# Optimization experiments

Hardware: AMD Instinct MI355X
Metric: run time of the kernel (lower is better)

Reference implementation:

```python
import jax, jax.numpy as jnp
import numpy as np

N = 50000
E = 800000
IN_C = 128
HID = 128
HEADS = 4
NEG_SLOPE = 0.2


def setup_inputs() -> dict:
    key = jax.random.key(0)
    ks = jax.random.split(key, 10)
    out_c = HID // HEADS  # 32
    glorot = lambda k, shape: jax.random.normal(k, shape, jnp.float32) * np.sqrt(2.0 / (shape[0] + shape[-1]))
    return {
        "x": jax.random.normal(ks[0], (N, IN_C), jnp.float32),
        "edge_index": jax.random.randint(ks[1], (2, E), 0, N, jnp.int64),
        # layer 1: GATConv(IN_C, out_c, heads=4, concat=True)
        "W1": glorot(ks[2], (IN_C, HEADS * out_c)),
        "att_src1": glorot(ks[3], (HEADS, out_c)),
        "att_dst1": glorot(ks[4], (HEADS, out_c)),
        "b1": jnp.zeros((HID,), jnp.float32),
        # layer 2: GATConv(HID, HID, heads=1, concat=False)
        "W2": glorot(ks[5], (HID, HID)),
        "att_src2": glorot(ks[6], (1, HID)),
        "att_dst2": glorot(ks[7], (1, HID)),
        "b2": jnp.zeros((HID,), jnp.float32),
    }


def _gat_conv(x, src, dst, W, att_src, att_dst, bias, heads, out_c):
    n = x.shape[0]
    h = (x @ W).reshape(n, heads, out_c)                 # [N, H, C]
    a_src = jnp.einsum("nhc,hc->nh", h, att_src)          # [N, H]
    a_dst = jnp.einsum("nhc,hc->nh", h, att_dst)          # [N, H]
    e = jax.nn.leaky_relu(a_src[src] + a_dst[dst], NEG_SLOPE)  # [E, H]
    # segment softmax over incoming edges of each dst node
    m = jax.ops.segment_max(e, dst, num_segments=n)
    p = jnp.exp(e - m[dst])
    denom = jax.ops.segment_sum(p, dst, num_segments=n)
    alpha = p / (denom[dst] + 1e-16)                      # [E, H]
    msg = h[src] * alpha[:, :, None]                      # [E, H, C]
    out = jax.ops.segment_sum(msg, dst, num_segments=n)   # [N, H, C]
    return out.reshape(n, heads * out_c) + bias


def reference(x, edge_index, W1, att_src1, att_dst1, b1, W2, att_src2, att_dst2, b2):
    n = x.shape[0]
    # PyG GATConv default add_self_loops=True
    loop = jnp.arange(n, dtype=edge_index.dtype)
    src = jnp.concatenate([edge_index[0], loop])
    dst = jnp.concatenate([edge_index[1], loop])

    out_c = HID // HEADS
    h = _gat_conv(x, src, dst, W1, att_src1, att_dst1, b1, HEADS, out_c)
    h = jax.nn.elu(h)  # dropout is identity in eval mode
    out = _gat_conv(h, src, dst, W2, att_src2, att_dst2, b2, 1, HID)
    return out
```

## Files before the change

### kernel.cpp

```cpp
#include <hip/hip_runtime.h>
#include <hip/hip_bf16.h>
#include <math.h>


#define NEG_SLOPE 0.2f
#define NBLK 256

using bf16x8 = __attribute__((ext_vector_type(8))) short;
using f32x4  = __attribute__((ext_vector_type(4))) float;

__device__ inline unsigned short f2bf(float x) {
    union { float f; unsigned int u; } v; v.f = x;
    unsigned int b = v.u + 0x7fffu + ((v.u >> 16) & 1u);
    return (unsigned short)(b >> 16);
}
__device__ inline unsigned int pack2bf(float a, float b) {
    return (unsigned int)f2bf(a) | ((unsigned int)f2bf(b) << 16);
}
__device__ inline float bf_lo(unsigned int u) { return __uint_as_float(u << 16); }
__device__ inline float bf_hi(unsigned int u) { return __uint_as_float(u & 0xffff0000u); }

__device__ inline int excl_scan_256(int v, int* scratch4) {
    const int t = threadIdx.x, lane = t & 63, w = t >> 6;
    int incl = v;
#pragma unroll
    for (int o = 1; o < 64; o <<= 1) {
        int u = __shfl_up(incl, o, 64);
        if (lane >= o) incl += u;
    }
    if (lane == 63) scratch4[w] = incl;
    __syncthreads();
    int wb = 0;
#pragma unroll
    for (int k = 0; k < 4; ++k)
        if (k < w) wb += scratch4[k];
    __syncthreads();
    return wb + incl - v;
}

__global__ __launch_bounds__(256) void part_hist_prep(const int* __restrict__ ei,
                                                      int* __restrict__ hist,
                                                      int E, int NB, int epb,
                                                      const float* __restrict__ W1,
                                                      const float* __restrict__ W2,
                                                      unsigned short* __restrict__ WT1,
                                                      unsigned short* __restrict__ WT2) {
    const int t = threadIdx.x;
    if (blockIdx.x >= NBLK) {
        __shared__ float Wl[64][132];
        const float* W = (blockIdx.x - NBLK) ? W2 : W1;
        unsigned short* WT = (blockIdx.x - NBLK) ? WT2 : WT1;
        for (int p = 0; p < 2; ++p) {
            if (p) __syncthreads();
            for (int u = t; u < 2048; u += 256) {
                int row = u >> 5, ch = u & 31;
                float4 v = *(const float4*)(W + (size_t)(p * 64 + row) * 128 + ch * 4);
                Wl[row][ch * 4 + 0] = v.x; Wl[row][ch * 4 + 1] = v.y;
                Wl[row][ch * 4 + 2] = v.z; Wl[row][ch * 4 + 3] = v.w;
            }
            __syncthreads();
            for (int u = t; u < 2048; u += 256) {
                int c = u >> 4, kc = u & 15;
                uint2 o;
                o.x = pack2bf(Wl[kc * 4 + 0][c], Wl[kc * 4 + 1][c]);
                o.y = pack2bf(Wl[kc * 4 + 2][c], Wl[kc * 4 + 3][c]);
                *(uint2*)(WT + (size_t)c * 128 + p * 64 + kc * 4) = o;
            }
        }
        return;
    }
    __shared__ int h[256];
    h[t] = 0;
    __syncthreads();
    const int e0 = blockIdx.x * epb;
    const int e1 = min(e0 + epb, E);
    for (int e = e0 + t; e < e1; e += 256) atomicAdd(&h[ei[E + e] >> 8], 1);
    __syncthreads();
    if (t < NB) hist[t * NBLK + blockIdx.x] = h[t];
}

__global__ __launch_bounds__(256) void part_scan(int* __restrict__ hist,
                                                 int* __restrict__ btotal) {
    __shared__ int s4[4];
    const int b = blockIdx.x, t = threadIdx.x;
    const int v = hist[b * NBLK + t];
    const int ex = excl_scan_256(v, s4);
    hist[b * NBLK + t] = ex;
    if (t == 255) btotal[b] = ex + v;
}

__global__ __launch_bounds__(256) void part_scatter(const int* __restrict__ ei,
                                                    const int* __restrict__ hist,
                                                    const int* __restrict__ btotal,
                                                    unsigned int* __restrict__ part,
                                                    int E, int NB, int epb) {
    __shared__ int s4[4];
    __shared__ int cur[256];
    const int t = threadIdx.x;
    const int tv = (t < NB) ? btotal[t] : 0;
    const int pb = excl_scan_256(tv, s4);
    cur[t] = (t < NB) ? pb + hist[t * NBLK + blockIdx.x] : 0;
    __syncthreads();
    const int e0 = blockIdx.x * epb;
    const int e1 = min(e0 + epb, E);
    for (int e = e0 + t; e < e1; e += 256) {
        const int d = ei[E + e];
        const int s = ei[e];
        const int pos = atomicAdd(&cur[d >> 8], 1);
        part[pos] = (unsigned int)s | ((unsigned int)(d & 255) << 16);
    }
}

__global__ __launch_bounds__(256) void csr_build(const unsigned int* __restrict__ part,
                                                 const int* __restrict__ btotal,
                                                 int* __restrict__ offs,
                                                 int* __restrict__ csr,
                                                 int n, int NB, int E) {
    __shared__ int s4[4];
    __shared__ int cnt[256], curq[256];
    __shared__ int sPB, sPE, sCB;
    const int b = blockIdx.x, t = threadIdx.x;
    const int tv = (t < NB) ? btotal[t] : 0;
    const int nnt = (t < NB) ? max(0, min(256, n - t * 256)) : 0;
    const int e1 = excl_scan_256(tv, s4);
    const int e2 = excl_scan_256(tv + nnt, s4);
    if (t == b) { sPB = e1; sPE = e1 + tv; sCB = e2; }
    const int node = b * 256 + t;
    cnt[t] = (node < n) ? 1 : 0;
    __syncthreads();
    for (int i = sPB + t; i < sPE; i += 256) atomicAdd(&cnt[(part[i] >> 16) & 255], 1);
    __syncthreads();
    const int c = cnt[t];
    const int loc = excl_scan_256(c, s4);
    curq[t] = loc + ((node < n) ? 1 : 0);
    if (node < n) {
        offs[node] = sCB + loc;
        csr[sCB + loc] = node;
    }
    if (b == 0 && t == 0) offs[n] = E + n;
    __syncthreads();
    for (int i = sPB + t; i < sPE; i += 256) {
        const unsigned int u = part[i];
        const int pos = atomicAdd(&curq[(u >> 16) & 255], 1);
        csr[sCB + pos] = (int)(u & 0xffffu);
    }
}

template <int H, bool IN_F32>
__global__ __launch_bounds__(512) void gemm_att(const float* __restrict__ Xf,
                                                const unsigned short* __restrict__ Xb,
                                                const unsigned short* __restrict__ WTb,
                                                unsigned int* __restrict__ Yb,
                                                const float* __restrict__ att_s,
                                                const float* __restrict__ att_d,
                                                float* __restrict__ as_,
                                                float* __restrict__ ad_, int n) {
    __shared__ unsigned short XL[128 * 128];
    __shared__ unsigned short WL[128 * 128];
    const int tid = threadIdx.x;
    const int r0g = blockIdx.x * 128;
#pragma unroll
    for (int p = 0; p < 4; ++p) {
        int u = tid + 512 * p;
        int row = u >> 4, ch = u & 15;
        uint4 v = {0, 0, 0, 0};
        int gr = r0g + row;
        if (gr < n) {
            if constexpr (IN_F32) {
                const float4* xp = (const float4*)(Xf + (size_t)gr * 128 + ch * 8);
                float4 f0 = xp[0], f1 = xp[1];
                v.x = pack2bf(f0.x, f0.y); v.y = pack2bf(f0.z, f0.w);
                v.z = pack2bf(f1.x, f1.y); v.w = pack2bf(f1.z, f1.w);
            } else {
                v = *(const uint4*)(Xb + (size_t)gr * 128 + ch * 8);
            }
        }
        int byte = (ch * 16) ^ ((row & 7) << 4);
        *(uint4*)((char*)XL + row * 256 + byte) = v;
    }
#pragma unroll
    for (int p = 0; p < 4; ++p) {
        int u = tid + 512 * p;
        int c = u >> 4, ch = u & 15;
        uint4 v = *(const uint4*)(WTb + (size_t)c * 128 + ch * 8);
        int byte = (ch * 16) ^ ((c & 7) << 4);
        *(uint4*)((char*)WL + c * 256 + byte) = v;
    }
    __syncthreads();

    const int w = tid >> 6, lane = tid & 63;
    const int lr = lane & 15, lq = lane >> 4;
    const int swz = (lr & 7) << 4;
    f32x4 acc[8];
#pragma unroll
    for (int cf = 0; cf < 8; ++cf) acc[cf] = (f32x4){0.f, 0.f, 0.f, 0.f};

    const char* XB = (const char*)XL + (w * 16 + lr) * 256;
    const char* WB = (const char*)WL + lr * 256;
#pragma unroll
    for (int k4 = 0; k4 < 4; ++k4) {
        const int off = (k4 * 64 + lq * 16) ^ swz;
        bf16x8 a = *(const bf16x8*)(XB + off);
#pragma unroll
        for (int cf = 0; cf < 8; ++cf) {
            bf16x8 b = *(const bf16x8*)(WB + cf * 4096 + off);
            acc[cf] = __builtin_amdgcn_mfma_f32_16x16x32_bf16(a, b, acc[cf], 0, 0, 0);
        }
    }

#pragma unroll
    for (int r = 0; r < 4; ++r) {
        int grow = r0g + w * 16 + lq * 4 + r;
        if (grow < n) {
            uint4 o;
            o.x = pack2bf(acc[0][r], acc[1][r]);
            o.y = pack2bf(acc[2][r], acc[3][r]);
            o.z = pack2bf(acc[4][r], acc[5][r]);
            o.w = pack2bf(acc[6][r], acc[7][r]);
            *(uint4*)((unsigned short*)Yb + (size_t)grow * 128 + lr * 8) = o;
        }
    }

    if constexpr (H == 4) {
        float pa[4][4], pd[4][4];
#pragma unroll
        for (int h = 0; h < 4; ++h)
#pragma unroll
            for (int r = 0; r < 4; ++r) { pa[h][r] = 0.f; pd[h][r] = 0.f; }
#pragma unroll
        for (int cf = 0; cf < 8; ++cf) {
            const float ws = att_s[cf * 16 + lr];
            const float wd = att_d[cf * 16 + lr];
#pragma unroll
            for (int r = 0; r < 4; ++r) {
                pa[cf >> 1][r] = fmaf(acc[cf][r], ws, pa[cf >> 1][r]);
                pd[cf >> 1][r] = fmaf(acc[cf][r], wd, pd[cf >> 1][r]);
            }
        }
#pragma unroll
        for (int o = 1; o < 16; o <<= 1) {
#pragma unroll
            for (int h = 0; h < 4; ++h)
#pragma unroll
                for (int r = 0; r < 4; ++r) {
                    pa[h][r] += __shfl_xor(pa[h][r], o, 64);
                    pd[h][r] += __shfl_xor(pd[h][r], o, 64);
                }
        }
        const int h = lr & 3, r = lr >> 2;
        float va = 0.f, vd = 0.f;
#pragma unroll
        for (int hh = 0; hh < 4; ++hh)
#pragma unroll
            for (int rr = 0; rr < 4; ++rr)
                if (h == hh && r == rr) { va = pa[hh][rr]; vd = pd[hh][rr]; }
        const int node = r0g + w * 16 + lq * 4 + r;
        if (node < n) {
            as_[(size_t)node * 4 + h] = va;
            ad_[(size_t)node * 4 + h] = vd;
        }
    } else {
        float pa[4], pd[4];
#pragma unroll
        for (int r = 0; r < 4; ++r) { pa[r] = 0.f; pd[r] = 0.f; }
#pragma unroll
        for (int cf = 0; cf < 8; ++cf) {
            const float ws = att_s[cf * 16 + lr];
            const float wd = att_d[cf * 16 + lr];
#pragma unroll
            for (int r = 0; r < 4; ++r) {
                pa[r] = fmaf(acc[cf][r], ws, pa[r]);
                pd[r] = fmaf(acc[cf][r], wd, pd[r]);
            }
        }
#pragma unroll
        for (int o = 1; o < 16; o <<= 1) {
#pragma unroll
            for (int r = 0; r < 4; ++r) {
                pa[r] += __shfl_xor(pa[r], o, 64);
                pd[r] += __shfl_xor(pd[r], o, 64);
            }
        }
        const int r = lr & 3;
        float va = 0.f, vd = 0.f;
#pragma unroll
        for (int rr = 0; rr < 4; ++rr)
            if (r == rr) { va = pa[rr]; vd = pd[rr]; }
        const int node = r0g + w * 16 + lq * 4 + r;
        if (node < n && lr < 8) {
            if (lr < 4) as_[node] = va;
            else        ad_[node] = vd;
        }
    }
}

template <int H, bool DO_ELU, bool OUT_BF16>
__global__ __launch_bounds__(256) void gat_gather5(
    const int* __restrict__ csr, const int* __restrict__ offs,
    const float* __restrict__ as_, const float* __restrict__ ad_,
    const unsigned int* __restrict__ hb,
    const float* __restrict__ bias, float* __restrict__ outf,
    unsigned short* __restrict__ outb, int n)
{
    constexpr int PW = (H == 4) ? 8 : 2;
    __shared__ float plds[4][68][PW];
    const int node = (int)(((size_t)blockIdx.x * blockDim.x + threadIdx.x) >> 6);
    if (node >= n) return;
    const int lane = threadIdx.x & 63;
    const int w = threadIdx.x >> 6;
    const int hd = lane & 3;
    const int lane4 = lane * 4;
    const int col0 = ((2 * lane) & 7) * 16 + (lane >> 2);
    const int col1 = col0 + 16;
    const int start = offs[node];
    const int deg = offs[node + 1] - start;
    const char* hbp = (const char*)hb;
    const char* pb = (const char*)&plds[w][0][0] + ((H == 4) ? hd * 8 : 0);

    if (lane < 3) {
#pragma unroll
        for (int k = 0; k < PW; ++k) plds[w][64 + lane][k] = 0.f;
    }

    float adx = 0.f, ady = 0.f, adz = 0.f, adw = 0.f;
    if constexpr (H == 4) {
        const float4 adv = *(const float4*)(ad_ + (size_t)node * 4);
        adx = adv.x; ady = adv.y; adz = adv.z; adw = adv.w;
    } else {
        adx = ad_[node];
    }

    float2 acc = {0.f, 0.f};
    float dsx = 0.f, dsy = 0.f, dsz = 0.f, dsw = 0.f;

    for (int base = 0; base < deg; base += 64) {
        const int cnt = min(deg - base, 64);
        {
            const bool act = lane < cnt;
            const int s = act ? csr[start + base + lane] : 0;
            const float sf = __int_as_float(s << 8);
            if constexpr (H == 4) {
                const float4 a = ((const float4*)as_)[s];
                float e0 = a.x + adx; e0 = fmaxf(e0, NEG_SLOPE * e0);
                float e1 = a.y + ady; e1 = fmaxf(e1, NEG_SLOPE * e1);
                float e2 = a.z + adz; e2 = fmaxf(e2, NEG_SLOPE * e2);
                float e3 = a.w + adw; e3 = fmaxf(e3, NEG_SLOPE * e3);
                float p0 = act ? __expf(e0) : 0.f;
                float p1 = act ? __expf(e1) : 0.f;
                float p2 = act ? __expf(e2) : 0.f;
                float p3 = act ? __expf(e3) : 0.f;
                dsx += p0; dsy += p1; dsz += p2; dsw += p3;
                float4 w0 = {p0, sf, p1, sf};
                float4 w1 = {p2, sf, p3, sf};
                *(float4*)&plds[w][lane][0] = w0;
                *(float4*)&plds[w][lane][4] = w1;
            } else {
                float e0 = as_[s] + adx; e0 = fmaxf(e0, NEG_SLOPE * e0);
                float p = act ? __expf(e0) : 0.f;
                dsx += p;
                float2 ps = {p, sf};
                *(float2*)&plds[w][lane][0] = ps;
            }
        }
        asm volatile("s_waitcnt lgkmcnt(0)" ::: "memory");
        __builtin_amdgcn_sched_barrier(0);

        float pA, pB, pC;
        unsigned int hA, hB, hC;
#define PRELB(S, T)                                                              \
    {                                                                            \
        const float2 ps = *(const float2*)(pb + (size_t)(T) * (PW * 4));         \
        p##S = ps.x;                                                             \
        h##S = *(const unsigned int*)(hbp + (__float_as_int(ps.y) | lane4));     \
    }
#define CONSB(S)                                                                 \
    {                                                                            \
        acc.x = fmaf(p##S, bf_lo(h##S), acc.x);                                  \
        acc.y = fmaf(p##S, bf_hi(h##S), acc.y);                                  \
    }
        PRELB(A, 0)
        PRELB(B, 1)
        PRELB(C, 2)
        int t = 0;
        for (; t + 3 <= cnt; t += 3) {
            CONSB(A) PRELB(A, t + 3)
            CONSB(B) PRELB(B, t + 4)
            CONSB(C) PRELB(C, t + 5)
        }
        if (t < cnt)     CONSB(A)
        if (t + 1 < cnt) CONSB(B)
        if (t + 2 < cnt) CONSB(C)
#undef PRELB
#undef CONSB
    }

#pragma unroll
    for (int o = 1; o < 64; o <<= 1) {
        dsx += __shfl_xor(dsx, o, 64);
        if constexpr (H == 4) {
            dsy += __shfl_xor(dsy, o, 64);
            dsz += __shfl_xor(dsz, o, 64);
            dsw += __shfl_xor(dsw, o, 64);
        }
    }
    float ds;
    if constexpr (H == 4) ds = hd == 0 ? dsx : hd == 1 ? dsy : hd == 2 ? dsz : dsw;
    else                  ds = dsx;

    const float bvx = bias[col0], bvy = bias[col1];
    const float inv = 1.f / (ds + 1e-16f);
    float v0 = acc.x * inv + bvx;
    float v1 = acc.y * inv + bvy;
    if constexpr (DO_ELU) {
        v0 = v0 > 0.f ? v0 : __expf(v0) - 1.f;
        v1 = v1 > 0.f ? v1 : __expf(v1) - 1.f;
    }
    if constexpr (OUT_BF16) {
        unsigned short* o16 = outb + (size_t)node * 128;
        o16[col0] = f2bf(v0);
        o16[col1] = f2bf(v1);
    } else {
        float* o32 = outf + (size_t)node * 128;
        o32[col0] = v0;
        o32[col1] = v1;
    }
}

extern "C" void kernel_launch(void* const* d_in, const int* in_sizes, int n_in,
                              void* d_out, int out_size, void* d_ws, size_t ws_size,
                              hipStream_t stream) {
    const float* x        = (const float*)d_in[0];
    const int*   ei       = (const int*)d_in[1];
    const float* W1       = (const float*)d_in[2];
    const float* att_src1 = (const float*)d_in[3];
    const float* att_dst1 = (const float*)d_in[4];
    const float* b1       = (const float*)d_in[5];
    const float* W2       = (const float*)d_in[6];
    const float* att_src2 = (const float*)d_in[7];
    const float* att_dst2 = (const float*)d_in[8];
    const float* b2       = (const float*)d_in[9];

    const int n  = in_sizes[0] / 128;
    const int E  = in_sizes[1] / 2;
    const int ET = E + n;
    const int NB = (n + 255) >> 8;
    const int epb = (E + NBLK - 1) / NBLK;

    unsigned int*   ws32 = (unsigned int*)d_ws;
    unsigned int*   Yb   = ws32;
    unsigned int*   Bb   = Yb + (size_t)n * 64;
    unsigned short* WT1  = (unsigned short*)(Bb + (size_t)n * 64);
    unsigned short* WT2  = WT1 + 128 * 128;
    float*          as_  = (float*)(WT2 + 128 * 128);
    float*          ad_  = as_ + (size_t)n * 4;
    int*            offs = (int*)(ad_ + (size_t)n * 4);
    int*            csr  = offs + n + 1;
    unsigned int*   part = (unsigned int*)(csr + ET);
    int*            hist = (int*)(part + E);
    int*            btot = hist + (size_t)NB * NBLK;

    float* outf = (float*)d_out;

    part_hist_prep<<<NBLK + 2, 256, 0, stream>>>(ei, hist, E, NB, epb,
                                                 W1, W2, WT1, WT2);
    part_scan<<<NB, 256, 0, stream>>>(hist, btot);
    part_scatter<<<NBLK, 256, 0, stream>>>(ei, hist, btot, part, E, NB, epb);
    csr_build<<<NB, 256, 0, stream>>>(part, btot, offs, csr, n, NB, E);

    gemm_att<4, true><<<(n + 127) / 128, 512, 0, stream>>>(
        x, nullptr, WT1, Yb, att_src1, att_dst1, as_, ad_, n);
    gat_gather5<4, true, true><<<((size_t)n * 64 + 255) / 256, 256, 0, stream>>>(
        csr, offs, as_, ad_, Yb, b1, nullptr, (unsigned short*)Bb, n);

    gemm_att<1, false><<<(n + 127) / 128, 512, 0, stream>>>(
        nullptr, (const unsigned short*)Bb, WT2, Yb, att_src2, att_dst2, as_, ad_, n);
    gat_gather5<1, false, false><<<((size_t)n * 64 + 255) / 256, 256, 0, stream>>>(
        csr, offs, as_, ad_, Yb, b2, outf, nullptr, n);
}
```

Before: 240.7 us.

## Drop LDS staging in GEMM and gather two edges per wavefront with 8-byte loads

The projection GEMM no longer stages X and W tiles in shared memory. Each wave loads its A fragments straight from global memory (converting fp32 to bf16 inline) and B fragments from the transposed weight, with 64-row blocks of 256 threads. The gather kernel splits the wave into two halves that handle alternate edges, each lane loading 8 bytes (4 bf16 features) per edge, and the halves are combined with a cross-half shuffle at the end. This aims to cut LDS traffic and barriers in the GEMM and to halve the serial per-edge iterations in the gather, at the cost of redundant global W reads and an extra reduction.

```diff
diff --git a/kernel.cpp b/kernel.cpp
--- a/kernel.cpp
+++ b/kernel.cpp
@@ -147,7 +147,7 @@
 }
 
 template <int H, bool IN_F32>
-__global__ __launch_bounds__(512) void gemm_att(const float* __restrict__ Xf,
+__global__ __launch_bounds__(256) void gemm_att(const float* __restrict__ Xf,
                                                 const unsigned short* __restrict__ Xb,
                                                 const unsigned short* __restrict__ WTb,
                                                 unsigned int* __restrict__ Yb,
@@ -155,55 +155,35 @@
                                                 const float* __restrict__ att_d,
                                                 float* __restrict__ as_,
                                                 float* __restrict__ ad_, int n) {
-    __shared__ unsigned short XL[128 * 128];
-    __shared__ unsigned short WL[128 * 128];
     const int tid = threadIdx.x;
-    const int r0g = blockIdx.x * 128;
-#pragma unroll
-    for (int p = 0; p < 4; ++p) {
-        int u = tid + 512 * p;
-        int row = u >> 4, ch = u & 15;
-        uint4 v = {0, 0, 0, 0};
-        int gr = r0g + row;
-        if (gr < n) {
-            if constexpr (IN_F32) {
-                const float4* xp = (const float4*)(Xf + (size_t)gr * 128 + ch * 8);
-                float4 f0 = xp[0], f1 = xp[1];
-                v.x = pack2bf(f0.x, f0.y); v.y = pack2bf(f0.z, f0.w);
-                v.z = pack2bf(f1.x, f1.y); v.w = pack2bf(f1.z, f1.w);
-            } else {
-                v = *(const uint4*)(Xb + (size_t)gr * 128 + ch * 8);
-            }
-        }
-        int byte = (ch * 16) ^ ((row & 7) << 4);
-        *(uint4*)((char*)XL + row * 256 + byte) = v;
-    }
-#pragma unroll
-    for (int p = 0; p < 4; ++p) {
-        int u = tid + 512 * p;
-        int c = u >> 4, ch = u & 15;
-        uint4 v = *(const uint4*)(WTb + (size_t)c * 128 + ch * 8);
-        int byte = (ch * 16) ^ ((c & 7) << 4);
-        *(uint4*)((char*)WL + c * 256 + byte) = v;
-    }
-    __syncthreads();
-
     const int w = tid >> 6, lane = tid & 63;
     const int lr = lane & 15, lq = lane >> 4;
-    const int swz = (lr & 7) << 4;
+    const int r0g = blockIdx.x * 64;
+    const int row = r0g + w * 16 + lr;
+    const int rowc = min(row, n - 1);
+
     f32x4 acc[8];
 #pragma unroll
     for (int cf = 0; cf < 8; ++cf) acc[cf] = (f32x4){0.f, 0.f, 0.f, 0.f};
 
-    const char* XB = (const char*)XL + (w * 16 + lr) * 256;
-    const char* WB = (const char*)WL + lr * 256;
+    const char* bbase = (const char*)WTb + lr * 256 + lq * 16;
+    const char* abase = IN_F32 ? (const char*)Xf + (size_t)rowc * 512 + lq * 32
+                               : (const char*)Xb + (size_t)rowc * 256 + lq * 16;
 #pragma unroll
     for (int k4 = 0; k4 < 4; ++k4) {
-        const int off = (k4 * 64 + lq * 16) ^ swz;
-        bf16x8 a = *(const bf16x8*)(XB + off);
+        bf16x8 a;
+        if constexpr (IN_F32) {
+            float4 f0 = *(const float4*)(abase + k4 * 128);
+            float4 f1 = *(const float4*)(abase + k4 * 128 + 16);
+            uint4 ua = {pack2bf(f0.x, f0.y), pack2bf(f0.z, f0.w),
+                        pack2bf(f1.x, f1.y), pack2bf(f1.z, f1.w)};
+            a = *(bf16x8*)&ua;
+        } else {
+            a = *(const bf16x8*)(abase + k4 * 64);
+        }
 #pragma unroll
         for (int cf = 0; cf < 8; ++cf) {
-            bf16x8 b = *(const bf16x8*)(WB + cf * 4096 + off);
+            bf16x8 b = *(const bf16x8*)(bbase + cf * 4096 + k4 * 64);
             acc[cf] = __builtin_amdgcn_mfma_f32_16x16x32_bf16(a, b, acc[cf], 0, 0, 0);
         }
     }
@@ -295,7 +275,7 @@
 }
 
 template <int H, bool DO_ELU, bool OUT_BF16>
-__global__ __launch_bounds__(256) void gat_gather5(
+__global__ __launch_bounds__(256) void gat_gather6(
     const int* __restrict__ csr, const int* __restrict__ offs,
     const float* __restrict__ as_, const float* __restrict__ ad_,
     const unsigned int* __restrict__ hb,
@@ -303,23 +283,25 @@
     unsigned short* __restrict__ outb, int n)
 {
     constexpr int PW = (H == 4) ? 8 : 2;
-    __shared__ float plds[4][68][PW];
+    __shared__ float plds[4][72][PW];
     const int node = (int)(((size_t)blockIdx.x * blockDim.x + threadIdx.x) >> 6);
     if (node >= n) return;
     const int lane = threadIdx.x & 63;
     const int w = threadIdx.x >> 6;
-    const int hd = lane & 3;
-    const int lane4 = lane * 4;
-    const int col0 = ((2 * lane) & 7) * 16 + (lane >> 2);
-    const int col1 = col0 + 16;
+    const int cl = lane & 31;
+    const int eh = lane >> 5;
+    const int cl8 = cl * 8;
+    const int c00 = 64 * (cl & 1) + (cl >> 1);
     const int start = offs[node];
     const int deg = offs[node + 1] - start;
     const char* hbp = (const char*)hb;
-    const char* pb = (const char*)&plds[w][0][0] + ((H == 4) ? hd * 8 : 0);
-
-    if (lane < 3) {
-#pragma unroll
-        for (int k = 0; k < PW; ++k) plds[w][64 + lane][k] = 0.f;
+    const char* pbase = (const char*)&plds[w][0][0] + eh * (PW * 4)
+                        + ((H == 4) ? (cl & 1) * 16 : 0);
+
+    {
+        float4 z = {0.f, 0.f, 0.f, 0.f};
+        float4* pz = (float4*)&plds[w][0][0];
+        for (int k = lane; k < 18 * PW; k += 64) pz[k] = z;
     }
 
     float adx = 0.f, ady = 0.f, adz = 0.f, adw = 0.f;
@@ -330,12 +312,12 @@
         adx = ad_[node];
     }
 
-    float2 acc = {0.f, 0.f};
+    float acc0 = 0.f, acc1 = 0.f, acc2 = 0.f, acc3 = 0.f;
     float dsx = 0.f, dsy = 0.f, dsz = 0.f, dsw = 0.f;
 
     for (int base = 0; base < deg; base += 64) {
         const int cnt = min(deg - base, 64);
-        {
+        if (lane <= cnt) {
             const bool act = lane < cnt;
             const int s = act ? csr[start + base + lane] : 0;
             const float sf = __int_as_float(s << 8);
@@ -350,8 +332,8 @@
                 float p2 = act ? __expf(e2) : 0.f;
                 float p3 = act ? __expf(e3) : 0.f;
                 dsx += p0; dsy += p1; dsz += p2; dsw += p3;
-                float4 w0 = {p0, sf, p1, sf};
-                float4 w1 = {p2, sf, p3, sf};
+                float4 w0 = {p0, p1, sf, 0.f};
+                float4 w1 = {p2, p3, sf, 0.f};
                 *(float4*)&plds[w][lane][0] = w0;
                 *(float4*)&plds[w][lane][4] = w1;
             } else {
@@ -365,35 +347,48 @@
         asm volatile("s_waitcnt lgkmcnt(0)" ::: "memory");
         __builtin_amdgcn_sched_barrier(0);
 
-        float pA, pB, pC;
-        unsigned int hA, hB, hC;
-#define PRELB(S, T)                                                              \
+        const int cntp = (cnt + 1) >> 1;
+        float pA0, pA1, pB0, pB1, pC0, pC1;
+        uint2 hA, hB, hC;
+#define PRELQ(S, PT)                                                             \
     {                                                                            \
-        const float2 ps = *(const float2*)(pb + (size_t)(T) * (PW * 4));         \
-        p##S = ps.x;                                                             \
-        h##S = *(const unsigned int*)(hbp + (__float_as_int(ps.y) | lane4));     \
-    }
-#define CONSB(S)                                                                 \
+        float sfl;                                                               \
+        if constexpr (H == 4) {                                                  \
+            float4 q = *(const float4*)(pbase + (size_t)(PT) * 64);              \
+            p##S##0 = q.x; p##S##1 = q.y; sfl = q.z;                             \
+        } else {                                                                 \
+            float2 q = *(const float2*)(pbase + (size_t)(PT) * 16);              \
+            p##S##0 = q.x; p##S##1 = q.x; sfl = q.y;                             \
+        }                                                                        \
+        h##S = *(const uint2*)(hbp + (__float_as_int(sfl) | cl8));               \
+    }
+#define CONSQ(S)                                                                 \
     {                                                                            \
-        acc.x = fmaf(p##S, bf_lo(h##S), acc.x);                                  \
-        acc.y = fmaf(p##S, bf_hi(h##S), acc.y);                                  \
-    }
-        PRELB(A, 0)
-        PRELB(B, 1)
-        PRELB(C, 2)
+        acc0 = fmaf(p##S##0, bf_lo(h##S.x), acc0);                               \
+        acc1 = fmaf(p##S##0, bf_hi(h##S.x), acc1);                               \
+        acc2 = fmaf(p##S##1, bf_lo(h##S.y), acc2);                               \
+        acc3 = fmaf(p##S##1, bf_hi(h##S.y), acc3);                               \
+    }
+        PRELQ(A, 0)
+        PRELQ(B, 1)
+        PRELQ(C, 2)
         int t = 0;
-        for (; t + 3 <= cnt; t += 3) {
-            CONSB(A) PRELB(A, t + 3)
-            CONSB(B) PRELB(B, t + 4)
-            CONSB(C) PRELB(C, t + 5)
-        }
-        if (t < cnt)     CONSB(A)
-        if (t + 1 < cnt) CONSB(B)
-        if (t + 2 < cnt) CONSB(C)
-#undef PRELB
-#undef CONSB
-    }
-
+        for (; t + 3 <= cntp; t += 3) {
+            CONSQ(A) PRELQ(A, t + 3)
+            CONSQ(B) PRELQ(B, t + 4)
+            CONSQ(C) PRELQ(C, t + 5)
+        }
+        if (t < cntp)     CONSQ(A)
+        if (t + 1 < cntp) CONSQ(B)
+        if (t + 2 < cntp) CONSQ(C)
+#undef PRELQ
+#undef CONSQ
+    }
+
+    acc0 += __shfl_xor(acc0, 32, 64);
+    acc1 += __shfl_xor(acc1, 32, 64);
+    acc2 += __shfl_xor(acc2, 32, 64);
+    acc3 += __shfl_xor(acc3, 32, 64);
 #pragma unroll
     for (int o = 1; o < 64; o <<= 1) {
         dsx += __shfl_xor(dsx, o, 64);
@@ -403,26 +398,40 @@
             dsw += __shfl_xor(dsw, o, 64);
         }
     }
-    float ds;
-    if constexpr (H == 4) ds = hd == 0 ? dsx : hd == 1 ? dsy : hd == 2 ? dsz : dsw;
-    else                  ds = dsx;
-
-    const float bvx = bias[col0], bvy = bias[col1];
-    const float inv = 1.f / (ds + 1e-16f);
-    float v0 = acc.x * inv + bvx;
-    float v1 = acc.y * inv + bvy;
-    if constexpr (DO_ELU) {
-        v0 = v0 > 0.f ? v0 : __expf(v0) - 1.f;
-        v1 = v1 > 0.f ? v1 : __expf(v1) - 1.f;
-    }
-    if constexpr (OUT_BF16) {
-        unsigned short* o16 = outb + (size_t)node * 128;
-        o16[col0] = f2bf(v0);
-        o16[col1] = f2bf(v1);
-    } else {
-        float* o32 = outf + (size_t)node * 128;
-        o32[col0] = v0;
-        o32[col1] = v1;
+
+    if (lane < 32) {
+        float i0, i1;
+        if constexpr (H == 4) {
+            const float d0 = (cl & 1) ? dsz : dsx;
+            const float d1 = (cl & 1) ? dsw : dsy;
+            i0 = 1.f / (d0 + 1e-16f);
+            i1 = 1.f / (d1 + 1e-16f);
+        } else {
+            i0 = i1 = 1.f / (dsx + 1e-16f);
+        }
+        float v0 = acc0 * i0 + bias[c00];
+        float v1 = acc1 * i0 + bias[c00 + 16];
+        float v2 = acc2 * i1 + bias[c00 + 32];
+        float v3 = acc3 * i1 + bias[c00 + 48];
+        if constexpr (DO_ELU) {
+            v0 = v0 > 0.f ? v0 : __expf(v0) - 1.f;
+            v1 = v1 > 0.f ? v1 : __expf(v1) - 1.f;
+            v2 = v2 > 0.f ? v2 : __expf(v2) - 1.f;
+            v3 = v3 > 0.f ? v3 : __expf(v3) - 1.f;
+        }
+        if constexpr (OUT_BF16) {
+            unsigned short* o16 = outb + (size_t)node * 128;
+            o16[c00]      = f2bf(v0);
+            o16[c00 + 16] = f2bf(v1);
+            o16[c00 + 32] = f2bf(v2);
+            o16[c00 + 48] = f2bf(v3);
+        } else {
+            float* o32 = outf + (size_t)node * 128;
+            o32[c00]      = v0;
+            o32[c00 + 16] = v1;
+            o32[c00 + 32] = v2;
+            o32[c00 + 48] = v3;
+        }
     }
 }
 
@@ -467,13 +476,13 @@
     part_scatter<<<NBLK, 256, 0, stream>>>(ei, hist, btot, part, E, NB, epb);
     csr_build<<<NB, 256, 0, stream>>>(part, btot, offs, csr, n, NB, E);
 
-    gemm_att<4, true><<<(n + 127) / 128, 512, 0, stream>>>(
+    gemm_att<4, true><<<(n + 63) / 64, 256, 0, stream>>>(
         x, nullptr, WT1, Yb, att_src1, att_dst1, as_, ad_, n);
-    gat_gather5<4, true, true><<<((size_t)n * 64 + 255) / 256, 256, 0, stream>>>(
+    gat_gather6<4, true, true><<<((size_t)n * 64 + 255) / 256, 256, 0, stream>>>(
         csr, offs, as_, ad_, Yb, b1, nullptr, (unsigned short*)Bb, n);
 
-    gemm_att<1, false><<<(n + 127) / 128, 512, 0, stream>>>(
+    gemm_att<1, false><<<(n + 63) / 64, 256, 0, stream>>>(
         nullptr, (const unsigned short*)Bb, WT2, Yb, att_src2, att_dst2, as_, ad_, n);
-    gat_gather5<1, false, false><<<((size_t)n * 64 + 255) / 256, 256, 0, stream>>>(
+    gat_gather6<1, false, false><<<((size_t)n * 64 + 255) / 256, 256, 0, stream>>>(
         csr, offs, as_, ad_, Yb, b2, outf, nullptr, n);
 }
```

Result: no change. 245.1 us (+1.8%).
